# Performance work log

Hardware: AMD Instinct MI355X
Metric: run time of the kernel (lower is better)

## Reference

```python
import jax, jax.numpy as jnp
import numpy as np

B, C, N = 8, 512, 2048
C8 = C // 8


def setup_inputs() -> dict:
    key = jax.random.key(0)
    ks = jax.random.split(key, 8)
    s = 1.0 / np.sqrt(C)
    return {
        "x": jax.random.normal(ks[0], (B, C, N, 1, 1), jnp.float32),
        "y": jax.random.normal(ks[1], (B, C, N, 1, 1), jnp.float32),
        "Wq": jax.random.normal(ks[2], (C8, C), jnp.float32) * s,
        "bq": jax.random.normal(ks[3], (C8,), jnp.float32) * s,
        "Wk": jax.random.normal(ks[4], (C8, C), jnp.float32) * s,
        "bk": jax.random.normal(ks[5], (C8,), jnp.float32) * s,
        "Wv": jax.random.normal(ks[6], (C, C), jnp.float32) * s,
        "bv": jax.random.normal(ks[7], (C,), jnp.float32) * s,
        "gamma": jnp.zeros((1,), jnp.float32),
    }


def reference(x, y, Wq, bq, Wk, bk, Wv, bv, gamma):
    xs = x[..., 0, 0]  # [B, C, N]
    ys = y[..., 0, 0]  # [B, C, N]
    # 1x1 Conv1d == channel-wise linear
    q = jnp.einsum('oc,bcn->bon', Wq, ys) + bq[None, :, None]  # [B, C8, N]
    k = jnp.einsum('oc,bcn->bon', Wk, xs) + bk[None, :, None]  # [B, C8, N]
    v = jnp.einsum('oc,bcn->bon', Wv, ys) + bv[None, :, None]  # [B, C, N]
    energy = jnp.einsum('bon,bom->bnm', q, k)  # [B, Ny, Nx], unscaled
    attention = jax.nn.softmax(energy, axis=-1)
    # out[b,c,n] = sum_m v[b,c,m] * attention[b,n,m]
    out = jnp.einsum('bcm,bnm->bcn', v, attention)
    out = gamma * out + xs
    return out[..., None, None], attention
```

## Files before the change

### kernel.cpp

```cpp
#include <hip/hip_runtime.h>

#define B_ 8
#define C_ 512
#define N_ 2048
#define C8_ 64

typedef short s16x8 __attribute__((ext_vector_type(8)));
typedef float f32x4 __attribute__((ext_vector_type(4)));

__device__ __forceinline__ ushort bf16_rne(float f) {
    unsigned u = __float_as_uint(f);
    u += 0x7FFFu + ((u >> 16) & 1u);
    return (ushort)(u >> 16);
}
__device__ __forceinline__ float bf16_to_f(ushort h) {
    return __uint_as_float((unsigned)h << 16);
}

__global__ __launch_bounds__(256) void wsplit_kernel(
    const float* __restrict__ Wq, const float* __restrict__ Wk,
    ushort* __restrict__ wqhi, ushort* __restrict__ wqlo,
    ushort* __restrict__ wkhi, ushort* __restrict__ wklo)
{
    int idx = blockIdx.x * 256 + threadIdx.x;
    if (idx >= 2 * C8_ * C_) return;
    bool isq = idx < C8_ * C_;
    int i = isq ? idx : idx - C8_ * C_;
    float f = isq ? Wq[i] : Wk[i];
    ushort h = bf16_rne(f);
    ushort l = bf16_rne(f - bf16_to_f(h));
    if (isq) { wqhi[i] = h; wqlo[i] = l; }
    else     { wkhi[i] = h; wklo[i] = l; }
}

__global__ __launch_bounds__(128) void qk_mfma_kernel(
    const ushort* __restrict__ whi, const ushort* __restrict__ wlo,
    const float* __restrict__ bias, const float* __restrict__ src,
    ushort* __restrict__ hi, ushort* __restrict__ lo)
{
    const int b  = blockIdx.x & 7;
    const int n0 = (blockIdx.x >> 3) * 32;
    const int w  = threadIdx.x >> 6;
    const int l  = threadIdx.x & 63;
    const int lc = l & 15;
    const int lq = l >> 4;
    const int nb = n0 + 16 * w;

    const float* ycol = src + (size_t)b * C_ * N_ + nb + lc;

    f32x4 acc[4];
    #pragma unroll
    for (int ot = 0; ot < 4; ++ot) acc[ot] = (f32x4){0.f, 0.f, 0.f, 0.f};

    #pragma unroll 4
    for (int ks = 0; ks < 16; ++ks) {
        const int c0 = ks * 32 + 8 * lq;
        float f[8];
        #pragma unroll
        for (int j = 0; j < 8; ++j)
            f[j] = ycol[(size_t)(c0 + j) * N_];
        ushort ah[8], al[8];
        #pragma unroll
        for (int j = 0; j < 8; ++j) {
            ah[j] = bf16_rne(f[j]);
            al[j] = bf16_rne(f[j] - bf16_to_f(ah[j]));
        }
        s16x8 ahi, alo;
        #pragma unroll
        for (int j = 0; j < 8; ++j) { ahi[j] = (short)ah[j]; alo[j] = (short)al[j]; }

        #pragma unroll
        for (int ot = 0; ot < 4; ++ot) {
            const size_t boff = (size_t)(ot * 16 + lc) * C_ + ks * 32 + 8 * lq;
            s16x8 bhi = *(const s16x8*)(whi + boff);
            s16x8 blo = *(const s16x8*)(wlo + boff);
            f32x4 c = acc[ot];
            c = __builtin_amdgcn_mfma_f32_16x16x32_bf16(ahi, bhi, c, 0, 0, 0);
            c = __builtin_amdgcn_mfma_f32_16x16x32_bf16(ahi, blo, c, 0, 0, 0);
            c = __builtin_amdgcn_mfma_f32_16x16x32_bf16(alo, bhi, c, 0, 0, 0);
            acc[ot] = c;
        }
    }

    #pragma unroll
    for (int ot = 0; ot < 4; ++ot) {
        const int o = ot * 16 + lc;
        const float bs = bias[o];
        #pragma unroll
        for (int i = 0; i < 4; ++i) {
            float v = acc[ot][i] + bs;
            ushort h = bf16_rne(v);
            ushort s = bf16_rne(v - bf16_to_f(h));
            size_t addr = ((size_t)b * N_ + nb + lq * 4 + i) * C8_ + o;
            hi[addr] = h;
            lo[addr] = s;
        }
    }
}

__global__ __launch_bounds__(512, 4) void attn_kernel(
    const ushort* __restrict__ qhi, const ushort* __restrict__ qlo,
    const ushort* __restrict__ khi, const ushort* __restrict__ klo,
    float* __restrict__ att)
{
    const int b  = blockIdx.x & 7;
    const int n0 = (blockIdx.x >> 3) * 16;
    const int t  = threadIdx.x;
    const int w  = t >> 6;
    const int l  = t & 63;
    const int lc = l & 15;
    const int lq = l >> 4;

    const size_t abase = ((size_t)b * N_ + n0 + lc) * C8_ + 8 * lq;
    const s16x8* qhp = (const s16x8*)(qhi + abase);
    const s16x8* qlp = (const s16x8*)(qlo + abase);
    s16x8 ah0 = qhp[0], ah1 = qhp[4];
    s16x8 al0 = qlp[0], al1 = qlp[4];

    const size_t bbase = ((size_t)b * N_ + w * 256 + lc) * C8_ + 8 * lq;

    f32x4 acc[16];
    #pragma unroll
    for (int i = 0; i < 16; ++i) acc[i] = (f32x4){0.f, 0.f, 0.f, 0.f};

    #pragma unroll
    for (int ti = 0; ti < 16; ++ti) {
        const s16x8* bh = (const s16x8*)(khi + bbase + (size_t)ti * 16 * C8_);
        const s16x8* bl = (const s16x8*)(klo + bbase + (size_t)ti * 16 * C8_);
        s16x8 bh0 = bh[0], bh1 = bh[4];
        s16x8 bl0 = bl[0], bl1 = bl[4];
        f32x4 c = acc[ti];
        c = __builtin_amdgcn_mfma_f32_16x16x32_bf16(ah0, bh0, c, 0, 0, 0);
        c = __builtin_amdgcn_mfma_f32_16x16x32_bf16(ah1, bh1, c, 0, 0, 0);
        c = __builtin_amdgcn_mfma_f32_16x16x32_bf16(ah0, bl0, c, 0, 0, 0);
        c = __builtin_amdgcn_mfma_f32_16x16x32_bf16(ah1, bl1, c, 0, 0, 0);
        c = __builtin_amdgcn_mfma_f32_16x16x32_bf16(al0, bh0, c, 0, 0, 0);
        c = __builtin_amdgcn_mfma_f32_16x16x32_bf16(al1, bh1, c, 0, 0, 0);
        acc[ti] = c;
    }

    #pragma unroll
    for (int ti = 0; ti < 16; ++ti)
        #pragma unroll
        for (int i = 0; i < 4; ++i)
            acc[ti][i] = __expf(acc[ti][i]);

    __shared__ float redsum[16][8];
    float ssum[4];
    #pragma unroll
    for (int i = 0; i < 4; ++i) {
        float s = 0.f;
        #pragma unroll
        for (int ti = 0; ti < 16; ++ti) s += acc[ti][i];
        #pragma unroll
        for (int off = 1; off < 16; off <<= 1)
            s += __shfl_xor(s, off, 64);
        ssum[i] = s;
    }
    if (lc == 0) {
        #pragma unroll
        for (int i = 0; i < 4; ++i) redsum[lq * 4 + i][w] = ssum[i];
    }
    __syncthreads();
    #pragma unroll
    for (int i = 0; i < 4; ++i) {
        float s = redsum[lq * 4 + i][0];
        #pragma unroll
        for (int ww = 1; ww < 8; ++ww) s += redsum[lq * 4 + i][ww];
        float inv = 1.0f / s;
        float* rowp = att + ((size_t)b * N_ + n0 + lq * 4 + i) * N_ + w * 256 + lc;
        #pragma unroll
        for (int ti = 0; ti < 16; ++ti)
            rowp[ti * 16] = acc[ti][i] * inv;
    }
}

__global__ __launch_bounds__(256) void v_kernel(
    const float* __restrict__ Wv, const float* __restrict__ bv,
    const float* __restrict__ y, const float* __restrict__ gamma,
    float* __restrict__ v)
{
    if (gamma[0] == 0.0f) return;
    const size_t total = (size_t)B_ * C_ * N_;
    for (size_t idx = (size_t)blockIdx.x * 256 + threadIdx.x; idx < total;
         idx += (size_t)gridDim.x * 256) {
        int n = (int)(idx % N_);
        int o = (int)((idx / N_) % C_);
        int b = (int)(idx / ((size_t)N_ * C_));
        float s = bv[o];
        for (int c = 0; c < C_; ++c)
            s += Wv[o * C_ + c] * y[((size_t)b * C_ + c) * N_ + n];
        v[idx] = s;
    }
}

__global__ __launch_bounds__(256) void out_kernel(
    const float* __restrict__ x, const float* __restrict__ gamma,
    const float* __restrict__ v, const float* __restrict__ att,
    float* __restrict__ out)
{
    const float g = gamma[0];
    size_t i = (size_t)blockIdx.x * blockDim.x + threadIdx.x;
    const float4* x4 = (const float4*)x;
    float4* o4 = (float4*)out;
    float4 xv = x4[i];
    if (g == 0.0f) {
        o4[i] = xv;
    } else {
        size_t base = i * 4;
        int n = (int)(base % N_);
        int cch = (int)((base / N_) % C_);
        int b = (int)(base / ((size_t)N_ * C_));
        const float* vp = v + ((size_t)b * C_ + cch) * N_;
        const float* a0 = att + ((size_t)b * N_ + n) * N_;
        float s0 = 0.f, s1 = 0.f, s2 = 0.f, s3 = 0.f;
        for (int m = 0; m < N_; ++m) {
            float vv = vp[m];
            s0 += vv * a0[m];
            s1 += vv * a0[(size_t)N_ + m];
            s2 += vv * a0[2 * (size_t)N_ + m];
            s3 += vv * a0[3 * (size_t)N_ + m];
        }
        o4[i] = make_float4(g * s0 + xv.x, g * s1 + xv.y, g * s2 + xv.z, g * s3 + xv.w);
    }
}

extern "C" void kernel_launch(void* const* d_in, const int* in_sizes, int n_in,
                              void* d_out, int out_size, void* d_ws, size_t ws_size,
                              hipStream_t stream)
{
    const float* x     = (const float*)d_in[0];
    const float* y     = (const float*)d_in[1];
    const float* Wq    = (const float*)d_in[2];
    const float* bq    = (const float*)d_in[3];
    const float* Wk    = (const float*)d_in[4];
    const float* bk    = (const float*)d_in[5];
    const float* Wv    = (const float*)d_in[6];
    const float* bv    = (const float*)d_in[7];
    const float* gamma = (const float*)d_in[8];

    float* out = (float*)d_out;
    float* att = (float*)d_out + (size_t)B_ * C_ * N_;

    char* ws = (char*)d_ws;
    ushort* wqhi = (ushort*)(ws);
    ushort* wqlo = (ushort*)(ws + (64u << 10));
    ushort* wkhi = (ushort*)(ws + (128u << 10));
    ushort* wklo = (ushort*)(ws + (192u << 10));
    ushort* qhi  = (ushort*)(ws + (1u << 20));
    ushort* qlo  = (ushort*)(ws + (3u << 20));
    ushort* khi  = (ushort*)(ws + (5u << 20));
    ushort* klo  = (ushort*)(ws + (7u << 20));
    float*  vbuf = (float*) (ws + (9u << 20));

    wsplit_kernel<<<(2 * C8_ * C_ + 255) / 256, 256, 0, stream>>>(
        Wq, Wk, wqhi, wqlo, wkhi, wklo);

    qk_mfma_kernel<<<512, 128, 0, stream>>>(wqhi, wqlo, bq, y, qhi, qlo);
    qk_mfma_kernel<<<512, 128, 0, stream>>>(wkhi, wklo, bk, x, khi, klo);

    attn_kernel<<<1024, 512, 0, stream>>>(qhi, qlo, khi, klo, att);

    v_kernel<<<4096, 256, 0, stream>>>(Wv, bv, y, gamma, vbuf);
    out_kernel<<<(B_ * C_ * N_ / 4) / 256, 256, 0, stream>>>(x, gamma, vbuf, att, out);
}
```

Baseline: 316.7 us.

## Merge Q/K projection launches and fuse gamma-zero residual copy into attention

Merges the two Q/K projection launches into one grid of 1024 blocks that picks its operands by block index. When gamma is zero, the residual copy of x into out moves into the attention kernel, and the separate out kernel returns early. v_kernel and out_kernel use smaller grid-stride grids, and 64-bit index arithmetic becomes 32-bit unsigned to cut address computation. The aim is fewer launches and better overlap of the copy with the attention writes, at the cost of extra per-block work in attn_kernel.

After: 318.4 us. No clear change (+0.5%).

```diff
diff --git a/kernel.cpp b/kernel.cpp
--- a/kernel.cpp
+++ b/kernel.cpp
@@ -34,19 +34,32 @@
 }
 
 __global__ __launch_bounds__(128) void qk_mfma_kernel(
-    const ushort* __restrict__ whi, const ushort* __restrict__ wlo,
-    const float* __restrict__ bias, const float* __restrict__ src,
-    ushort* __restrict__ hi, ushort* __restrict__ lo)
-{
-    const int b  = blockIdx.x & 7;
-    const int n0 = (blockIdx.x >> 3) * 32;
+    const ushort* __restrict__ wqhi, const ushort* __restrict__ wqlo,
+    const float* __restrict__ bq,  const float* __restrict__ ysrc,
+    const ushort* __restrict__ wkhi, const ushort* __restrict__ wklo,
+    const float* __restrict__ bk,  const float* __restrict__ xsrc,
+    ushort* __restrict__ qhi, ushort* __restrict__ qlo,
+    ushort* __restrict__ khi, ushort* __restrict__ klo)
+{
+    const int bid = blockIdx.x;
+    const int id  = bid & 511;
+    const bool isq = bid < 512;
+    const ushort* __restrict__ whi  = isq ? wqhi : wkhi;
+    const ushort* __restrict__ wlo  = isq ? wqlo : wklo;
+    const float*  __restrict__ bias = isq ? bq : bk;
+    const float*  __restrict__ src  = isq ? ysrc : xsrc;
+    ushort* __restrict__ hi = isq ? qhi : khi;
+    ushort* __restrict__ lo = isq ? qlo : klo;
+
+    const int b  = id & 7;
+    const int n0 = (id >> 3) * 32;
     const int w  = threadIdx.x >> 6;
     const int l  = threadIdx.x & 63;
     const int lc = l & 15;
     const int lq = l >> 4;
     const int nb = n0 + 16 * w;
 
-    const float* ycol = src + (size_t)b * C_ * N_ + nb + lc;
+    const float* ycol = src + ((unsigned)b * C_ * N_ + nb + lc);
 
     f32x4 acc[4];
     #pragma unroll
@@ -58,7 +71,7 @@
         float f[8];
         #pragma unroll
         for (int j = 0; j < 8; ++j)
-            f[j] = ycol[(size_t)(c0 + j) * N_];
+            f[j] = ycol[(unsigned)(c0 + j) * N_];
         ushort ah[8], al[8];
         #pragma unroll
         for (int j = 0; j < 8; ++j) {
@@ -71,7 +84,7 @@
 
         #pragma unroll
         for (int ot = 0; ot < 4; ++ot) {
-            const size_t boff = (size_t)(ot * 16 + lc) * C_ + ks * 32 + 8 * lq;
+            const unsigned boff = (unsigned)(ot * 16 + lc) * C_ + ks * 32 + 8 * lq;
             s16x8 bhi = *(const s16x8*)(whi + boff);
             s16x8 blo = *(const s16x8*)(wlo + boff);
             f32x4 c = acc[ot];
@@ -91,7 +104,7 @@
             float v = acc[ot][i] + bs;
             ushort h = bf16_rne(v);
             ushort s = bf16_rne(v - bf16_to_f(h));
-            size_t addr = ((size_t)b * N_ + nb + lq * 4 + i) * C8_ + o;
+            unsigned addr = ((unsigned)b * N_ + nb + lq * 4 + i) * C8_ + o;
             hi[addr] = h;
             lo[addr] = s;
         }
@@ -101,7 +114,9 @@
 __global__ __launch_bounds__(512, 4) void attn_kernel(
     const ushort* __restrict__ qhi, const ushort* __restrict__ qlo,
     const ushort* __restrict__ khi, const ushort* __restrict__ klo,
-    float* __restrict__ att)
+    float* __restrict__ att,
+    const float* __restrict__ x, const float* __restrict__ gamma,
+    float* __restrict__ out)
 {
     const int b  = blockIdx.x & 7;
     const int n0 = (blockIdx.x >> 3) * 16;
@@ -111,13 +126,13 @@
     const int lc = l & 15;
     const int lq = l >> 4;
 
-    const size_t abase = ((size_t)b * N_ + n0 + lc) * C8_ + 8 * lq;
+    const unsigned abase = ((unsigned)b * N_ + n0 + lc) * C8_ + 8 * lq;
     const s16x8* qhp = (const s16x8*)(qhi + abase);
     const s16x8* qlp = (const s16x8*)(qlo + abase);
     s16x8 ah0 = qhp[0], ah1 = qhp[4];
     s16x8 al0 = qlp[0], al1 = qlp[4];
 
-    const size_t bbase = ((size_t)b * N_ + w * 256 + lc) * C8_ + 8 * lq;
+    const unsigned bbase = ((unsigned)b * N_ + w * 256 + lc) * C8_ + 8 * lq;
 
     f32x4 acc[16];
     #pragma unroll
@@ -125,8 +140,8 @@
 
     #pragma unroll
     for (int ti = 0; ti < 16; ++ti) {
-        const s16x8* bh = (const s16x8*)(khi + bbase + (size_t)ti * 16 * C8_);
-        const s16x8* bl = (const s16x8*)(klo + bbase + (size_t)ti * 16 * C8_);
+        const s16x8* bh = (const s16x8*)(khi + bbase + (unsigned)ti * 16 * C8_);
+        const s16x8* bl = (const s16x8*)(klo + bbase + (unsigned)ti * 16 * C8_);
         s16x8 bh0 = bh[0], bh1 = bh[4];
         s16x8 bl0 = bl[0], bl1 = bl[4];
         f32x4 c = acc[ti];
@@ -168,10 +183,20 @@
         #pragma unroll
         for (int ww = 1; ww < 8; ++ww) s += redsum[lq * 4 + i][ww];
         float inv = 1.0f / s;
-        float* rowp = att + ((size_t)b * N_ + n0 + lq * 4 + i) * N_ + w * 256 + lc;
+        float* rowp = att + ((unsigned)b * N_ + n0 + lq * 4 + i) * N_ + w * 256 + lc;
         #pragma unroll
         for (int ti = 0; ti < 16; ++ti)
             rowp[ti * 16] = acc[ti][i] * inv;
+    }
+
+    if (gamma[0] == 0.0f) {
+        #pragma unroll
+        for (int p = 0; p < 4; ++p) {
+            const int c = p * 128 + (t >> 2);
+            const int j = t & 3;
+            const unsigned off = ((unsigned)b * C_ + c) * N_ + n0 + 4 * j;
+            *(float4*)(out + off) = *(const float4*)(x + off);
+        }
     }
 }
 
@@ -200,13 +225,13 @@
     float* __restrict__ out)
 {
     const float g = gamma[0];
-    size_t i = (size_t)blockIdx.x * blockDim.x + threadIdx.x;
+    if (g == 0.0f) return;
+    const size_t nf4 = (size_t)B_ * C_ * N_ / 4;
     const float4* x4 = (const float4*)x;
     float4* o4 = (float4*)out;
-    float4 xv = x4[i];
-    if (g == 0.0f) {
-        o4[i] = xv;
-    } else {
+    for (size_t i = (size_t)blockIdx.x * blockDim.x + threadIdx.x; i < nf4;
+         i += (size_t)gridDim.x * blockDim.x) {
+        float4 xv = x4[i];
         size_t base = i * 4;
         int n = (int)(base % N_);
         int cch = (int)((base / N_) % C_);
@@ -256,11 +281,11 @@
     wsplit_kernel<<<(2 * C8_ * C_ + 255) / 256, 256, 0, stream>>>(
         Wq, Wk, wqhi, wqlo, wkhi, wklo);
 
-    qk_mfma_kernel<<<512, 128, 0, stream>>>(wqhi, wqlo, bq, y, qhi, qlo);
-    qk_mfma_kernel<<<512, 128, 0, stream>>>(wkhi, wklo, bk, x, khi, klo);
-
-    attn_kernel<<<1024, 512, 0, stream>>>(qhi, qlo, khi, klo, att);
-
-    v_kernel<<<4096, 256, 0, stream>>>(Wv, bv, y, gamma, vbuf);
-    out_kernel<<<(B_ * C_ * N_ / 4) / 256, 256, 0, stream>>>(x, gamma, vbuf, att, out);
-}
+    qk_mfma_kernel<<<1024, 128, 0, stream>>>(
+        wqhi, wqlo, bq, y, wkhi, wklo, bk, x, qhi, qlo, khi, klo);
+
+    attn_kernel<<<1024, 512, 0, stream>>>(qhi, qlo, khi, klo, att, x, gamma, out);
+
+    v_kernel<<<1024, 256, 0, stream>>>(Wv, bv, y, gamma, vbuf);
+    out_kernel<<<2048, 256, 0, stream>>>(x, gamma, vbuf, att, out);
+}
```
